# Optimization experiments

Hardware: AMD Instinct MI355X
Metric: run time of the kernel (lower is better)

## Reference

```python
import jax, jax.numpy as jnp
import numpy as np

NEG_SLOPE = 0.2


def gat_conv(x, src, dst, W, a_src, a_dst, bias, heads, out_ch):
    """PyG-style GATConv (concat=True, self-loops already appended)."""
    N = x.shape[0]
    h = (x @ W).reshape(N, heads, out_ch)            # [N,H,C]
    al_s = jnp.einsum('nhc,hc->nh', h, a_src)        # [N,H]
    al_d = jnp.einsum('nhc,hc->nh', h, a_dst)        # [N,H]
    e = al_s[src] + al_d[dst]                        # [E,H]
    e = jnp.where(e > 0, e, NEG_SLOPE * e)           # leaky_relu
    # segment softmax over edges grouped by destination node
    m = jax.ops.segment_max(e, dst, num_segments=N)  # [N,H]
    ex = jnp.exp(e - m[dst])
    s = jax.ops.segment_sum(ex, dst, num_segments=N)
    alpha = ex / s[dst]                              # [E,H]
    msg = alpha[:, :, None] * h[src]                 # [E,H,C]
    out = jax.ops.segment_sum(msg, dst, num_segments=N)  # [N,H,C]
    return out.reshape(N, heads * out_ch) + bias


def setup_inputs() -> dict:
    key = jax.random.key(0)
    ks = jax.random.split(key, 10)
    N, E = 100000, 1600000
    return {
        'x': jax.random.normal(ks[0], (N, 4), dtype=jnp.float32),
        'edge_index': jax.random.randint(ks[1], (2, E), 0, N, dtype=jnp.int64),
        'W1': jax.random.normal(ks[2], (4, 32), dtype=jnp.float32) * 0.5,
        'a_src1': jax.random.normal(ks[3], (2, 16), dtype=jnp.float32) * 0.5,
        'a_dst1': jax.random.normal(ks[4], (2, 16), dtype=jnp.float32) * 0.5,
        'b1': jax.random.normal(ks[5], (32,), dtype=jnp.float32) * 0.1,
        'W2': jax.random.normal(ks[6], (32, 2), dtype=jnp.float32) * 0.2,
        'a_src2': jax.random.normal(ks[7], (1, 2), dtype=jnp.float32) * 0.5,
        'a_dst2': jax.random.normal(ks[8], (1, 2), dtype=jnp.float32) * 0.5,
        'b2': jax.random.normal(ks[9], (2,), dtype=jnp.float32) * 0.1,
    }


def reference(x, edge_index, W1, a_src1, a_dst1, b1, W2, a_src2, a_dst2, b2):
    N = x.shape[0]
    loop = jnp.arange(N, dtype=edge_index.dtype)     # add_self_loops=True
    src = jnp.concatenate([edge_index[0], loop])
    dst = jnp.concatenate([edge_index[1], loop])
    # dropout(p=0.6) is identity at inference
    h = gat_conv(x, src, dst, W1, a_src1, a_dst1, b1, heads=2, out_ch=16)
    h = jax.nn.elu(h)
    out = gat_conv(h, src, dst, W2, a_src2, a_dst2, b2, heads=1, out_ch=2)
    return out
```

## Files before the change

### kernel.cpp

```cpp
#include <hip/hip_runtime.h>
#include <hip/hip_fp16.h>
#include <math.h>

#define NEG_SLOPE 0.2f
#define SCAN_CHUNK 2048
#define ECLAMP 80.0f
#define BUCKET_SHIFT 8
#define BUCKET_MASK 255
#define EB_CHUNK 8192

__device__ __forceinline__ float lrelu(float e) {
    return e > 0.f ? e : NEG_SLOPE * e;
}

__global__ void k0_prep1(const float* __restrict__ x,
                         const float* __restrict__ W1,
                         const float* __restrict__ a_src1,
                         const float* __restrict__ a_dst1,
                         __half* __restrict__ h1,
                         float* __restrict__ as1,
                         float* __restrict__ ad1,
                         int N) {
    int t = blockIdx.x * blockDim.x + threadIdx.x;
    int n = t >> 5;
    int c = t & 31;
    if (n >= N) return;
    const float4 xv = reinterpret_cast<const float4*>(x)[n];
    float h = xv.x * W1[c] + xv.y * W1[32 + c] + xv.z * W1[64 + c] + xv.w * W1[96 + c];
    h1[n * 32 + c] = __float2half(h);
    float ts = h * a_src1[c];
    float td = h * a_dst1[c];
#pragma unroll
    for (int m = 8; m >= 1; m >>= 1) {
        ts += __shfl_xor(ts, m);
        td += __shfl_xor(td, m);
    }
    if ((c & 15) == 0) {
        int hh = c >> 4;
        as1[n * 2 + hh] = ts;
        ad1[n * 2 + hh] = td;
    }
}

__global__ void p1_hist(const int* __restrict__ dst, int* __restrict__ cmatT,
                        int E, int NB, int nblkE) {
    __shared__ int cnt[512];
    const int blk = blockIdx.x, tid = threadIdx.x;
    for (int b = tid; b < NB; b += 256) cnt[b] = 0;
    __syncthreads();
    int base = blk * EB_CHUNK;
    int end = min(base + EB_CHUNK, E);
    for (int e = base + tid; e < end; e += 256)
        atomicAdd(&cnt[dst[e] >> BUCKET_SHIFT], 1);
    __syncthreads();
    for (int b = tid; b < NB; b += 256)
        cmatT[(size_t)b * nblkE + blk] = cnt[b];
}

__global__ void k2a_partials(const int* __restrict__ in, int* __restrict__ bsum, int n) {
    __shared__ int ws[4];
    const int tid = threadIdx.x;
    const int lane = tid & 63, wid = tid >> 6;
    int base = blockIdx.x * SCAN_CHUNK + tid * 8;
    int lsum = 0;
#pragma unroll
    for (int i = 0; i < 8; ++i) {
        int idx = base + i;
        lsum += (idx < n) ? in[idx] : 0;
    }
#pragma unroll
    for (int m = 32; m >= 1; m >>= 1) lsum += __shfl_xor(lsum, m);
    if (lane == 0) ws[wid] = lsum;
    __syncthreads();
    if (tid == 0) bsum[blockIdx.x] = ws[0] + ws[1] + ws[2] + ws[3];
}

__global__ void k2b_scanb(const int* __restrict__ bsum, int* __restrict__ bscan, int nb) {
    __shared__ int wsum[16];
    const int tid = threadIdx.x;
    const int lane = tid & 63, wid = tid >> 6;
    int carry = 0;
    for (int base = 0; base < nb; base += 1024) {
        int i = base + tid;
        int v = (i < nb) ? bsum[i] : 0;
        int xx = v;
#pragma unroll
        for (int off = 1; off < 64; off <<= 1) {
            int t = __shfl_up(xx, off);
            if (lane >= off) xx += t;
        }
        if (lane == 63) wsum[wid] = xx;
        __syncthreads();
        int woff = 0;
        for (int w = 0; w < wid; ++w) woff += wsum[w];
        if (i < nb) bscan[i] = carry + woff + xx - v;
        int tot = 0;
        for (int w = 0; w < 16; ++w) tot += wsum[w];
        carry += tot;
        __syncthreads();
    }
}

__global__ void k2c_scan(const int* __restrict__ in, const int* __restrict__ bscan,
                         int* __restrict__ out, int n) {
    __shared__ int ws[4];
    const int tid = threadIdx.x;
    const int lane = tid & 63, wid = tid >> 6;
    int base = blockIdx.x * SCAN_CHUNK + tid * 8;
    int v[8], pre[8];
    int lsum = 0;
#pragma unroll
    for (int i = 0; i < 8; ++i) {
        int idx = base + i;
        v[i] = (idx < n) ? in[idx] : 0;
        pre[i] = lsum;
        lsum += v[i];
    }
    int xs = lsum;
#pragma unroll
    for (int off = 1; off < 64; off <<= 1) {
        int t = __shfl_up(xs, off);
        if (lane >= off) xs += t;
    }
    if (lane == 63) ws[wid] = xs;
    __syncthreads();
    int woff = 0;
    for (int w = 0; w < wid; ++w) woff += ws[w];
    int off0 = bscan[blockIdx.x] + woff + xs - lsum;
#pragma unroll
    for (int i = 0; i < 8; ++i) {
        int idx = base + i;
        if (idx < n) out[idx] = off0 + pre[i];
    }
}

__global__ void p3_scatter(const int* __restrict__ src, const int* __restrict__ dst,
                           const int* __restrict__ cscan, unsigned int* __restrict__ ebuf,
                           int E, int NB, int nblkE) {
    __shared__ int cur[512];
    const int blk = blockIdx.x, tid = threadIdx.x;
    for (int b = tid; b < NB; b += 256)
        cur[b] = cscan[(size_t)b * nblkE + blk];
    __syncthreads();
    int base = blk * EB_CHUNK;
    int end = min(base + EB_CHUNK, E);
    for (int e = base + tid; e < end; e += 256) {
        int d = dst[e];
        int b = d >> BUCKET_SHIFT;
        int pos = atomicAdd(&cur[b], 1);
        ebuf[pos] = (unsigned int)src[e] | ((unsigned int)(d & BUCKET_MASK) << 24);
    }
}

__global__ void p4_csr(const unsigned int* __restrict__ ebuf,
                       const int* __restrict__ cscan,
                       int* __restrict__ rp, int* __restrict__ esrt,
                       int N, int E, int NB, int nblkE) {
    __shared__ int degl[256];
    __shared__ int curl[256];
    __shared__ int wsum[4];
    const int b = blockIdx.x, tid = threadIdx.x;
    const int lane = tid & 63, wid = tid >> 6;
    int bstart = cscan[(size_t)b * nblkE];
    int bend = (b + 1 < NB) ? cscan[(size_t)(b + 1) * nblkE] : E;
    degl[tid] = 0;
    __syncthreads();
    for (int i = bstart + tid; i < bend; i += 256)
        atomicAdd(&degl[ebuf[i] >> 24], 1);
    __syncthreads();
    int v = degl[tid];
    int xs = v;
#pragma unroll
    for (int off = 1; off < 64; off <<= 1) {
        int t = __shfl_up(xs, off);
        if (lane >= off) xs += t;
    }
    if (lane == 63) wsum[wid] = xs;
    __syncthreads();
    int woff = 0;
    for (int w = 0; w < wid; ++w) woff += wsum[w];
    int excl = woff + xs - v;
    int node = (b << BUCKET_SHIFT) + tid;
    if (node < N) rp[node] = bstart + excl;
    curl[tid] = bstart + excl;
    if (b == 0 && tid == 0) rp[N] = E;
    __syncthreads();
    for (int i = bstart + tid; i < bend; i += 256) {
        unsigned int ev = ebuf[i];
        int dl = ev >> 24;
        int pos = atomicAdd(&curl[dl], 1);
        esrt[pos] = (int)(ev & 0x00FFFFFFu);
    }
}

__global__ void k4_layer1(const int* __restrict__ rp, const int* __restrict__ esrt,
                          const __half* __restrict__ h1, const float* __restrict__ as1,
                          const float* __restrict__ ad1, const float* __restrict__ b1,
                          const float* __restrict__ W2, const float* __restrict__ a_src2,
                          const float* __restrict__ a_dst2,
                          float4* __restrict__ h2p, float* __restrict__ ad2,
                          int N) {
    int t = blockIdx.x * blockDim.x + threadIdx.x;
    int n = t >> 5;
    int c = t & 31;
    if (n >= N) return;
    int hh = c >> 4;
    const float2* as1v = reinterpret_cast<const float2*>(as1);
    const float2* ad1v = reinterpret_cast<const float2*>(ad1);
    float2 adv = ad1v[n];
    float ad = hh ? adv.y : adv.x;
    float2 asv_self = as1v[n];
    float e_self = lrelu((hh ? asv_self.y : asv_self.x) + ad);
    float w_self = __expf(fminf(e_self, ECLAMP));
    float s0 = w_self, s1 = 0.f, s2 = 0.f, s3 = 0.f;
    float acc0 = w_self * __half2float(h1[n * 32 + c]);
    float acc1 = 0.f, acc2 = 0.f, acc3 = 0.f;

    int p0 = rp[n], p1 = rp[n + 1];
    int p = p0;
    for (; p + 3 < p1; p += 4) {
        int sa = esrt[p];
        int sb = esrt[p + 1];
        int sc_ = esrt[p + 2];
        int sd = esrt[p + 3];
        float2 va = as1v[sa];
        float2 vb = as1v[sb];
        float2 vc = as1v[sc_];
        float2 vd = as1v[sd];
        float ha = __half2float(h1[(size_t)sa * 32 + c]);
        float hb = __half2float(h1[(size_t)sb * 32 + c]);
        float hc = __half2float(h1[(size_t)sc_ * 32 + c]);
        float hd = __half2float(h1[(size_t)sd * 32 + c]);
        float pa = __expf(fminf(lrelu((hh ? va.y : va.x) + ad), ECLAMP));
        float pb = __expf(fminf(lrelu((hh ? vb.y : vb.x) + ad), ECLAMP));
        float pc = __expf(fminf(lrelu((hh ? vc.y : vc.x) + ad), ECLAMP));
        float pd = __expf(fminf(lrelu((hh ? vd.y : vd.x) + ad), ECLAMP));
        s0 += pa;   acc0 += pa * ha;
        s1 += pb;   acc1 += pb * hb;
        s2 += pc;   acc2 += pc * hc;
        s3 += pd;   acc3 += pd * hd;
    }
    for (; p < p1; ++p) {
        int sa = esrt[p];
        float2 va = as1v[sa];
        float ha = __half2float(h1[(size_t)sa * 32 + c]);
        float pa = __expf(fminf(lrelu((hh ? va.y : va.x) + ad), ECLAMP));
        s0 += pa;   acc0 += pa * ha;
    }
    float s = (s0 + s1) + (s2 + s3);
    float acc = (acc0 + acc1) + (acc2 + acc3);
    float o = acc / s + b1[c];
    o = o > 0.f ? o : expm1f(o);
    float t0 = o * W2[c * 2 + 0];
    float t1 = o * W2[c * 2 + 1];
#pragma unroll
    for (int msk = 16; msk >= 1; msk >>= 1) {
        t0 += __shfl_xor(t0, msk);
        t1 += __shfl_xor(t1, msk);
    }
    if (c == 0) {
        float as2v = t0 * a_src2[0] + t1 * a_src2[1];
        float ad2v = t0 * a_dst2[0] + t1 * a_dst2[1];
        h2p[n] = make_float4(t0, t1, as2v, 0.f);
        ad2[n] = ad2v;
    }
}

__global__ void k5_layer2(const int* __restrict__ rp, const int* __restrict__ esrt,
                          const float4* __restrict__ h2p, const float* __restrict__ ad2,
                          const float* __restrict__ b2,
                          float* __restrict__ out, int N) {
    int t = blockIdx.x * blockDim.x + threadIdx.x;
    int n = t >> 2;
    int sub = t & 3;
    if (n >= N) return;
    float ad = ad2[n];
    float s = 0.f, xx = 0.f, yy = 0.f;
    if (sub == 0) {
        float4 hv = h2p[n];
        float w = __expf(fminf(lrelu(hv.z + ad), ECLAMP));
        s = w; xx = w * hv.x; yy = w * hv.y;
    }
    int p0 = rp[n], p1 = rp[n + 1];
    for (int p = p0 + sub; p < p1; p += 4) {
        int sn = esrt[p];
        float4 hv = h2p[sn];
        float w = __expf(fminf(lrelu(hv.z + ad), ECLAMP));
        s += w; xx += w * hv.x; yy += w * hv.y;
    }
#pragma unroll
    for (int msk = 1; msk <= 2; msk <<= 1) {
        s  += __shfl_xor(s, msk);
        xx += __shfl_xor(xx, msk);
        yy += __shfl_xor(yy, msk);
    }
    if (sub == 0) {
        float2 o;
        o.x = xx / s + b2[0];
        o.y = yy / s + b2[1];
        reinterpret_cast<float2*>(out)[n] = o;
    }
}

extern "C" void kernel_launch(void* const* d_in, const int* in_sizes, int n_in,
                              void* d_out, int out_size, void* d_ws, size_t ws_size,
                              hipStream_t stream) {
    const float* x      = (const float*)d_in[0];
    const int*   ei     = (const int*)d_in[1];
    const float* W1     = (const float*)d_in[2];
    const float* a_src1 = (const float*)d_in[3];
    const float* a_dst1 = (const float*)d_in[4];
    const float* b1     = (const float*)d_in[5];
    const float* W2     = (const float*)d_in[6];
    const float* a_src2 = (const float*)d_in[7];
    const float* a_dst2 = (const float*)d_in[8];
    const float* b2     = (const float*)d_in[9];
    float* out = (float*)d_out;

    const int N = in_sizes[0] / 4;
    const int E = in_sizes[1] / 2;
    const int* srcp = ei;
    const int* dstp = ei + E;

    const int NB    = (N + BUCKET_MASK) >> BUCKET_SHIFT;
    const int nblkE = (E + EB_CHUNK - 1) / EB_CHUNK;
    const int M     = NB * nblkE;
    const int nb2   = (M + SCAN_CHUNK - 1) / SCAN_CHUNK;

    char* w = (char*)d_ws;
    __half* h1   = (__half*)w;  w += (size_t)N * 32 * sizeof(__half);
    float*  as1  = (float*)w;   w += (size_t)N * 2 * sizeof(float);
    float*  ad1  = (float*)w;   w += (size_t)N * 2 * sizeof(float);
    float4* h2p  = (float4*)w;  w += (size_t)N * sizeof(float4);
    float*  ad2  = (float*)w;   w += (size_t)N * sizeof(float);
    int* rp     = (int*)w;      w += (size_t)(N + 4) * sizeof(int);
    int* cmatT  = (int*)w;      w += (size_t)M * sizeof(int);
    int* cscan  = (int*)w;      w += (size_t)M * sizeof(int);
    int* bsum   = (int*)w;      w += (size_t)(nb2 + 4) * sizeof(int);
    int* bscan  = (int*)w;      w += (size_t)(nb2 + 4) * sizeof(int);
    unsigned int* ebuf = (unsigned int*)w;  w += (size_t)E * sizeof(unsigned int);
    int* esrt   = (int*)w;      w += (size_t)E * sizeof(int);

    const int BT = 256;
    k0_prep1<<<((size_t)N * 32 + BT - 1) / BT, BT, 0, stream>>>(
        x, W1, a_src1, a_dst1, h1, as1, ad1, N);
    p1_hist<<<nblkE, 256, 0, stream>>>(dstp, cmatT, E, NB, nblkE);
    k2a_partials<<<nb2, 256, 0, stream>>>(cmatT, bsum, M);
    k2b_scanb<<<1, 1024, 0, stream>>>(bsum, bscan, nb2);
    k2c_scan<<<nb2, 256, 0, stream>>>(cmatT, bscan, cscan, M);
    p3_scatter<<<nblkE, 256, 0, stream>>>(srcp, dstp, cscan, ebuf, E, NB, nblkE);
    p4_csr<<<NB, 256, 0, stream>>>(ebuf, cscan, rp, esrt, N, E, NB, nblkE);
    k4_layer1<<<((size_t)N * 32 + BT - 1) / BT, BT, 0, stream>>>(
        rp, esrt, h1, as1, ad1, b1, W2, a_src2, a_dst2, h2p, ad2, N);
    k5_layer2<<<((size_t)N * 4 + BT - 1) / BT, BT, 0, stream>>>(
        rp, esrt, h2p, ad2, b2, out, N);
}
```

Before: 211.3 us.

## Precompute layer-1 softmax weights and node max/sum inside CSR build kernel

The CSR bucket kernel now computes the per-edge attention logits for layer 1, takes a per-destination max with ordered-int atomics in shared memory, and stores fp16 exp weights per edge plus per-node max and sum. The layer-1 aggregation kernel then reads these precomputed weights instead of gathering as1 and evaluating exp 32 times per edge (once per channel lane). This removes redundant exp and gather work from the hot kernel, but it adds a 4-byte weight array per edge, more shared-memory atomics and larger shared usage in p4_csr, and weights rounded to fp16.

Result: slower. 224.4 us (+6.2%).

```diff
diff --git a/kernel.cpp b/kernel.cpp
--- a/kernel.cpp
+++ b/kernel.cpp
@@ -4,13 +4,22 @@
 
 #define NEG_SLOPE 0.2f
 #define SCAN_CHUNK 2048
-#define ECLAMP 80.0f
 #define BUCKET_SHIFT 8
 #define BUCKET_MASK 255
 #define EB_CHUNK 8192
+#define EL_CAP 4992
+#define FENC_NEGINF 0x007FFFFFu
 
 __device__ __forceinline__ float lrelu(float e) {
     return e > 0.f ? e : NEG_SLOPE * e;
+}
+__device__ __forceinline__ unsigned fenc(float f) {
+    unsigned u = __float_as_uint(f);
+    return (u & 0x80000000u) ? ~u : (u | 0x80000000u);
+}
+__device__ __forceinline__ float fdec(unsigned u) {
+    unsigned b = (u & 0x80000000u) ? (u & 0x7FFFFFFFu) : ~u;
+    return __uint_as_float(b);
 }
 
 __global__ void k0_prep1(const float* __restrict__ x,
@@ -154,19 +163,46 @@
 
 __global__ void p4_csr(const unsigned int* __restrict__ ebuf,
                        const int* __restrict__ cscan,
+                       const float* __restrict__ as1,
+                       const float* __restrict__ ad1,
                        int* __restrict__ rp, int* __restrict__ esrt,
+                       __half2* __restrict__ wgtH, float4* __restrict__ nst,
                        int N, int E, int NB, int nblkE) {
+    __shared__ float2 eL[EL_CAP];
+    __shared__ unsigned maxL[512];
+    __shared__ float ssumL[512];
     __shared__ int degl[256];
     __shared__ int curl[256];
+    __shared__ float2 adL[256];
     __shared__ int wsum[4];
     const int b = blockIdx.x, tid = threadIdx.x;
     const int lane = tid & 63, wid = tid >> 6;
+    const float2* as1v = reinterpret_cast<const float2*>(as1);
+    const float2* ad1v = reinterpret_cast<const float2*>(ad1);
     int bstart = cscan[(size_t)b * nblkE];
     int bend = (b + 1 < NB) ? cscan[(size_t)(b + 1) * nblkE] : E;
+    int node = (b << BUCKET_SHIFT) + tid;
     degl[tid] = 0;
-    __syncthreads();
-    for (int i = bstart + tid; i < bend; i += 256)
-        atomicAdd(&degl[ebuf[i] >> 24], 1);
+    maxL[tid] = FENC_NEGINF;
+    maxL[tid + 256] = FENC_NEGINF;
+    ssumL[tid] = 0.f;
+    ssumL[tid + 256] = 0.f;
+    adL[tid] = (node < N) ? ad1v[node] : make_float2(0.f, 0.f);
+    __syncthreads();
+    for (int i = bstart + tid; i < bend; i += 256) {
+        unsigned ev = ebuf[i];
+        int dl = ev >> 24;
+        int srcn = ev & 0x00FFFFFF;
+        atomicAdd(&degl[dl], 1);
+        float2 av = as1v[srcn];
+        float2 adv = adL[dl];
+        float e0 = lrelu(av.x + adv.x);
+        float e1 = lrelu(av.y + adv.y);
+        int sl = i - bstart;
+        if (sl < EL_CAP) eL[sl] = make_float2(e0, e1);
+        atomicMax(&maxL[dl * 2], fenc(e0));
+        atomicMax(&maxL[dl * 2 + 1], fenc(e1));
+    }
     __syncthreads();
     int v = degl[tid];
     int xs = v;
@@ -180,20 +216,42 @@
     int woff = 0;
     for (int w = 0; w < wid; ++w) woff += wsum[w];
     int excl = woff + xs - v;
-    int node = (b << BUCKET_SHIFT) + tid;
     if (node < N) rp[node] = bstart + excl;
     curl[tid] = bstart + excl;
     if (b == 0 && tid == 0) rp[N] = E;
     __syncthreads();
     for (int i = bstart + tid; i < bend; i += 256) {
-        unsigned int ev = ebuf[i];
+        unsigned ev = ebuf[i];
         int dl = ev >> 24;
+        int srcn = ev & 0x00FFFFFF;
+        int sl = i - bstart;
+        float2 e;
+        if (sl < EL_CAP) {
+            e = eL[sl];
+        } else {
+            float2 av = as1v[srcn];
+            float2 adv = adL[dl];
+            e = make_float2(lrelu(av.x + adv.x), lrelu(av.y + adv.y));
+        }
+        float m0 = fdec(maxL[dl * 2]);
+        float m1 = fdec(maxL[dl * 2 + 1]);
+        float w0 = __expf(e.x - m0);
+        float w1 = __expf(e.y - m1);
+        atomicAdd(&ssumL[dl * 2], w0);
+        atomicAdd(&ssumL[dl * 2 + 1], w1);
         int pos = atomicAdd(&curl[dl], 1);
-        esrt[pos] = (int)(ev & 0x00FFFFFFu);
-    }
+        esrt[pos] = srcn;
+        wgtH[pos] = __floats2half2_rn(w0, w1);
+    }
+    __syncthreads();
+    if (node < N)
+        nst[node] = make_float4(fdec(maxL[tid * 2]), fdec(maxL[tid * 2 + 1]),
+                                ssumL[tid * 2], ssumL[tid * 2 + 1]);
 }
 
 __global__ void k4_layer1(const int* __restrict__ rp, const int* __restrict__ esrt,
+                          const __half2* __restrict__ wgtH,
+                          const float4* __restrict__ nst,
                           const __half* __restrict__ h1, const float* __restrict__ as1,
                           const float* __restrict__ ad1, const float* __restrict__ b1,
                           const float* __restrict__ W2, const float* __restrict__ a_src2,
@@ -208,48 +266,49 @@
     const float2* as1v = reinterpret_cast<const float2*>(as1);
     const float2* ad1v = reinterpret_cast<const float2*>(ad1);
     float2 adv = ad1v[n];
-    float ad = hh ? adv.y : adv.x;
-    float2 asv_self = as1v[n];
-    float e_self = lrelu((hh ? asv_self.y : asv_self.x) + ad);
-    float w_self = __expf(fminf(e_self, ECLAMP));
-    float s0 = w_self, s1 = 0.f, s2 = 0.f, s3 = 0.f;
-    float acc0 = w_self * __half2float(h1[n * 32 + c]);
-    float acc1 = 0.f, acc2 = 0.f, acc3 = 0.f;
-
+    float2 asv = as1v[n];
+    float es = lrelu((hh ? asv.y : asv.x) + (hh ? adv.y : adv.x));
+    float h_self = __half2float(h1[(size_t)n * 32 + c]);
+    float4 ns = nst[n];
     int p0 = rp[n], p1 = rp[n + 1];
-    int p = p0;
-    for (; p + 3 < p1; p += 4) {
-        int sa = esrt[p];
-        int sb = esrt[p + 1];
-        int sc_ = esrt[p + 2];
-        int sd = esrt[p + 3];
-        float2 va = as1v[sa];
-        float2 vb = as1v[sb];
-        float2 vc = as1v[sc_];
-        float2 vd = as1v[sd];
-        float ha = __half2float(h1[(size_t)sa * 32 + c]);
-        float hb = __half2float(h1[(size_t)sb * 32 + c]);
-        float hc = __half2float(h1[(size_t)sc_ * 32 + c]);
-        float hd = __half2float(h1[(size_t)sd * 32 + c]);
-        float pa = __expf(fminf(lrelu((hh ? va.y : va.x) + ad), ECLAMP));
-        float pb = __expf(fminf(lrelu((hh ? vb.y : vb.x) + ad), ECLAMP));
-        float pc = __expf(fminf(lrelu((hh ? vc.y : vc.x) + ad), ECLAMP));
-        float pd = __expf(fminf(lrelu((hh ? vd.y : vd.x) + ad), ECLAMP));
-        s0 += pa;   acc0 += pa * ha;
-        s1 += pb;   acc1 += pb * hb;
-        s2 += pc;   acc2 += pc * hc;
-        s3 += pd;   acc3 += pd * hd;
-    }
-    for (; p < p1; ++p) {
-        int sa = esrt[p];
-        float2 va = as1v[sa];
-        float ha = __half2float(h1[(size_t)sa * 32 + c]);
-        float pa = __expf(fminf(lrelu((hh ? va.y : va.x) + ad), ECLAMP));
-        s0 += pa;   acc0 += pa * ha;
-    }
-    float s = (s0 + s1) + (s2 + s3);
-    float acc = (acc0 + acc1) + (acc2 + acc3);
-    float o = acc / s + b1[c];
+    float acc, stot;
+    if (p0 == p1) {
+        acc = h_self;
+        stot = 1.f;
+    } else {
+        float m = hh ? ns.y : ns.x;
+        float se = hh ? ns.w : ns.z;
+        float w_self = __expf(es - m);
+        stot = se + w_self;
+        float a0 = w_self * h_self, a1 = 0.f, a2 = 0.f, a3 = 0.f;
+        int p = p0;
+        for (; p + 3 < p1; p += 4) {
+            int sa = esrt[p];
+            int sb = esrt[p + 1];
+            int sc_ = esrt[p + 2];
+            int sd = esrt[p + 3];
+            __half2 wa = wgtH[p];
+            __half2 wb = wgtH[p + 1];
+            __half2 wc = wgtH[p + 2];
+            __half2 wd = wgtH[p + 3];
+            float ha = __half2float(h1[(size_t)sa * 32 + c]);
+            float hb = __half2float(h1[(size_t)sb * 32 + c]);
+            float hc = __half2float(h1[(size_t)sc_ * 32 + c]);
+            float hd = __half2float(h1[(size_t)sd * 32 + c]);
+            a0 += (hh ? __high2float(wa) : __low2float(wa)) * ha;
+            a1 += (hh ? __high2float(wb) : __low2float(wb)) * hb;
+            a2 += (hh ? __high2float(wc) : __low2float(wc)) * hc;
+            a3 += (hh ? __high2float(wd) : __low2float(wd)) * hd;
+        }
+        for (; p < p1; ++p) {
+            int sa = esrt[p];
+            __half2 wa = wgtH[p];
+            float ha = __half2float(h1[(size_t)sa * 32 + c]);
+            a0 += (hh ? __high2float(wa) : __low2float(wa)) * ha;
+        }
+        acc = (a0 + a1) + (a2 + a3);
+    }
+    float o = acc / stot + b1[c];
     o = o > 0.f ? o : expm1f(o);
     float t0 = o * W2[c * 2 + 0];
     float t1 = o * W2[c * 2 + 1];
@@ -278,14 +337,14 @@
     float s = 0.f, xx = 0.f, yy = 0.f;
     if (sub == 0) {
         float4 hv = h2p[n];
-        float w = __expf(fminf(lrelu(hv.z + ad), ECLAMP));
+        float w = __expf(fminf(lrelu(hv.z + ad), 80.f));
         s = w; xx = w * hv.x; yy = w * hv.y;
     }
     int p0 = rp[n], p1 = rp[n + 1];
     for (int p = p0 + sub; p < p1; p += 4) {
         int sn = esrt[p];
         float4 hv = h2p[sn];
-        float w = __expf(fminf(lrelu(hv.z + ad), ECLAMP));
+        float w = __expf(fminf(lrelu(hv.z + ad), 80.f));
         s += w; xx += w * hv.x; yy += w * hv.y;
     }
 #pragma unroll
@@ -333,6 +392,7 @@
     float*  ad1  = (float*)w;   w += (size_t)N * 2 * sizeof(float);
     float4* h2p  = (float4*)w;  w += (size_t)N * sizeof(float4);
     float*  ad2  = (float*)w;   w += (size_t)N * sizeof(float);
+    float4* nst  = (float4*)w;  w += (size_t)N * sizeof(float4);
     int* rp     = (int*)w;      w += (size_t)(N + 4) * sizeof(int);
     int* cmatT  = (int*)w;      w += (size_t)M * sizeof(int);
     int* cscan  = (int*)w;      w += (size_t)M * sizeof(int);
@@ -340,6 +400,7 @@
     int* bscan  = (int*)w;      w += (size_t)(nb2 + 4) * sizeof(int);
     unsigned int* ebuf = (unsigned int*)w;  w += (size_t)E * sizeof(unsigned int);
     int* esrt   = (int*)w;      w += (size_t)E * sizeof(int);
+    __half2* wgtH = (__half2*)w; w += (size_t)E * sizeof(__half2);
 
     const int BT = 256;
     k0_prep1<<<((size_t)N * 32 + BT - 1) / BT, BT, 0, stream>>>(
@@ -349,9 +410,10 @@
     k2b_scanb<<<1, 1024, 0, stream>>>(bsum, bscan, nb2);
     k2c_scan<<<nb2, 256, 0, stream>>>(cmatT, bscan, cscan, M);
     p3_scatter<<<nblkE, 256, 0, stream>>>(srcp, dstp, cscan, ebuf, E, NB, nblkE);
-    p4_csr<<<NB, 256, 0, stream>>>(ebuf, cscan, rp, esrt, N, E, NB, nblkE);
+    p4_csr<<<NB, 256, 0, stream>>>(ebuf, cscan, as1, ad1, rp, esrt, wgtH, nst,
+                                   N, E, NB, nblkE);
     k4_layer1<<<((size_t)N * 32 + BT - 1) / BT, BT, 0, stream>>>(
-        rp, esrt, h1, as1, ad1, b1, W2, a_src2, a_dst2, h2p, ad2, N);
+        rp, esrt, wgtH, nst, h1, as1, ad1, b1, W2, a_src2, a_dst2, h2p, ad2, N);
     k5_layer2<<<((size_t)N * 4 + BT - 1) / BT, BT, 0, stream>>>(
         rp, esrt, h2p, ad2, b2, out, N);
 }
```

## Aggregate raw 4-dim inputs in layer 1 and apply W1 after aggregation

Applied to the files above, without the earlier changes.

Uses linearity: since h = xW1, the attention-weighted sum of h[src] equals W1 applied to the weighted sum of x[src]. Layer 1 now gathers 4-float x rows per head instead of 32-wide fp16 h1 rows, runs 8 threads per node instead of 32, and no longer materialises h1 in the prep kernel. This cuts gather traffic and thread count in the dominant edge loop. The cost is a small per-node matmul after aggregation and a slightly different rounding order.

Result: faster. 179.2 us (-15.2%).

```diff
diff --git a/kernel.cpp b/kernel.cpp
--- a/kernel.cpp
+++ b/kernel.cpp
@@ -1,5 +1,4 @@
 #include <hip/hip_runtime.h>
-#include <hip/hip_fp16.h>
 #include <math.h>
 
 #define NEG_SLOPE 0.2f
@@ -17,7 +16,6 @@
                          const float* __restrict__ W1,
                          const float* __restrict__ a_src1,
                          const float* __restrict__ a_dst1,
-                         __half* __restrict__ h1,
                          float* __restrict__ as1,
                          float* __restrict__ ad1,
                          int N) {
@@ -27,7 +25,6 @@
     if (n >= N) return;
     const float4 xv = reinterpret_cast<const float4*>(x)[n];
     float h = xv.x * W1[c] + xv.y * W1[32 + c] + xv.z * W1[64 + c] + xv.w * W1[96 + c];
-    h1[n * 32 + c] = __float2half(h);
     float ts = h * a_src1[c];
     float td = h * a_dst1[c];
 #pragma unroll
@@ -194,27 +191,24 @@
 }
 
 __global__ void k4_layer1(const int* __restrict__ rp, const int* __restrict__ esrt,
-                          const __half* __restrict__ h1, const float* __restrict__ as1,
+                          const float* __restrict__ x, const float* __restrict__ as1,
                           const float* __restrict__ ad1, const float* __restrict__ b1,
+                          const float* __restrict__ W1,
                           const float* __restrict__ W2, const float* __restrict__ a_src2,
                           const float* __restrict__ a_dst2,
                           float4* __restrict__ h2p, float* __restrict__ ad2,
                           int N) {
     int t = blockIdx.x * blockDim.x + threadIdx.x;
-    int n = t >> 5;
-    int c = t & 31;
+    int n = t >> 3;
+    int l = t & 7;
     if (n >= N) return;
-    int hh = c >> 4;
-    const float2* as1v = reinterpret_cast<const float2*>(as1);
-    const float2* ad1v = reinterpret_cast<const float2*>(ad1);
-    float2 adv = ad1v[n];
-    float ad = hh ? adv.y : adv.x;
-    float2 asv_self = as1v[n];
-    float e_self = lrelu((hh ? asv_self.y : asv_self.x) + ad);
-    float w_self = __expf(fminf(e_self, ECLAMP));
-    float s0 = w_self, s1 = 0.f, s2 = 0.f, s3 = 0.f;
-    float acc0 = w_self * __half2float(h1[n * 32 + c]);
-    float acc1 = 0.f, acc2 = 0.f, acc3 = 0.f;
+    int h = l >> 2;
+    int d = l & 3;
+    float ad = ad1[n * 2 + h];
+    float es = lrelu(as1[n * 2 + h] + ad);
+    float ws = __expf(fminf(es, ECLAMP));
+    float g0 = ws * x[(size_t)n * 4 + d], g1 = 0.f, g2 = 0.f, g3 = 0.f;
+    float s0 = ws, s1 = 0.f, s2 = 0.f, s3 = 0.f;
 
     int p0 = rp[n], p1 = rp[n + 1];
     int p = p0;
@@ -223,42 +217,58 @@
         int sb = esrt[p + 1];
         int sc_ = esrt[p + 2];
         int sd = esrt[p + 3];
-        float2 va = as1v[sa];
-        float2 vb = as1v[sb];
-        float2 vc = as1v[sc_];
-        float2 vd = as1v[sd];
-        float ha = __half2float(h1[(size_t)sa * 32 + c]);
-        float hb = __half2float(h1[(size_t)sb * 32 + c]);
-        float hc = __half2float(h1[(size_t)sc_ * 32 + c]);
-        float hd = __half2float(h1[(size_t)sd * 32 + c]);
-        float pa = __expf(fminf(lrelu((hh ? va.y : va.x) + ad), ECLAMP));
-        float pb = __expf(fminf(lrelu((hh ? vb.y : vb.x) + ad), ECLAMP));
-        float pc = __expf(fminf(lrelu((hh ? vc.y : vc.x) + ad), ECLAMP));
-        float pd = __expf(fminf(lrelu((hh ? vd.y : vd.x) + ad), ECLAMP));
-        s0 += pa;   acc0 += pa * ha;
-        s1 += pb;   acc1 += pb * hb;
-        s2 += pc;   acc2 += pc * hc;
-        s3 += pd;   acc3 += pd * hd;
+        float ea = lrelu(as1[(size_t)sa * 2 + h] + ad);
+        float eb = lrelu(as1[(size_t)sb * 2 + h] + ad);
+        float ec = lrelu(as1[(size_t)sc_ * 2 + h] + ad);
+        float ed = lrelu(as1[(size_t)sd * 2 + h] + ad);
+        float xa = x[(size_t)sa * 4 + d];
+        float xb = x[(size_t)sb * 4 + d];
+        float xc = x[(size_t)sc_ * 4 + d];
+        float xd = x[(size_t)sd * 4 + d];
+        float wa = __expf(fminf(ea, ECLAMP));
+        float wb = __expf(fminf(eb, ECLAMP));
+        float wc = __expf(fminf(ec, ECLAMP));
+        float wd = __expf(fminf(ed, ECLAMP));
+        s0 += wa;  g0 += wa * xa;
+        s1 += wb;  g1 += wb * xb;
+        s2 += wc;  g2 += wc * xc;
+        s3 += wd;  g3 += wd * xd;
     }
     for (; p < p1; ++p) {
         int sa = esrt[p];
-        float2 va = as1v[sa];
-        float ha = __half2float(h1[(size_t)sa * 32 + c]);
-        float pa = __expf(fminf(lrelu((hh ? va.y : va.x) + ad), ECLAMP));
-        s0 += pa;   acc0 += pa * ha;
+        float ea = lrelu(as1[(size_t)sa * 2 + h] + ad);
+        float xa = x[(size_t)sa * 4 + d];
+        float wa = __expf(fminf(ea, ECLAMP));
+        s0 += wa;  g0 += wa * xa;
     }
     float s = (s0 + s1) + (s2 + s3);
-    float acc = (acc0 + acc1) + (acc2 + acc3);
-    float o = acc / s + b1[c];
-    o = o > 0.f ? o : expm1f(o);
-    float t0 = o * W2[c * 2 + 0];
-    float t1 = o * W2[c * 2 + 1];
-#pragma unroll
-    for (int msk = 16; msk >= 1; msk >>= 1) {
+    float agg = ((g0 + g1) + (g2 + g3)) / s;
+
+    float a2[2][4];
+#pragma unroll
+    for (int k = 0; k < 8; ++k)
+        a2[k >> 2][k & 3] = __shfl(agg, k, 8);
+
+    float t0 = 0.f, t1 = 0.f;
+#pragma unroll
+    for (int j = 0; j < 4; ++j) {
+        int c = l * 4 + j;
+        int hc = c >> 4;
+        float o = b1[c]
+                + a2[hc][0] * W1[c]
+                + a2[hc][1] * W1[32 + c]
+                + a2[hc][2] * W1[64 + c]
+                + a2[hc][3] * W1[96 + c];
+        o = o > 0.f ? o : expm1f(o);
+        t0 += o * W2[c * 2 + 0];
+        t1 += o * W2[c * 2 + 1];
+    }
+#pragma unroll
+    for (int msk = 1; msk <= 4; msk <<= 1) {
         t0 += __shfl_xor(t0, msk);
         t1 += __shfl_xor(t1, msk);
     }
-    if (c == 0) {
+    if (l == 0) {
         float as2v = t0 * a_src2[0] + t1 * a_src2[1];
         float ad2v = t0 * a_dst2[0] + t1 * a_dst2[1];
         h2p[n] = make_float4(t0, t1, as2v, 0.f);
@@ -328,10 +338,9 @@
     const int nb2   = (M + SCAN_CHUNK - 1) / SCAN_CHUNK;
 
     char* w = (char*)d_ws;
-    __half* h1   = (__half*)w;  w += (size_t)N * 32 * sizeof(__half);
+    float4* h2p  = (float4*)w;  w += (size_t)N * sizeof(float4);
     float*  as1  = (float*)w;   w += (size_t)N * 2 * sizeof(float);
     float*  ad1  = (float*)w;   w += (size_t)N * 2 * sizeof(float);
-    float4* h2p  = (float4*)w;  w += (size_t)N * sizeof(float4);
     float*  ad2  = (float*)w;   w += (size_t)N * sizeof(float);
     int* rp     = (int*)w;      w += (size_t)(N + 4) * sizeof(int);
     int* cmatT  = (int*)w;      w += (size_t)M * sizeof(int);
@@ -343,15 +352,15 @@
 
     const int BT = 256;
     k0_prep1<<<((size_t)N * 32 + BT - 1) / BT, BT, 0, stream>>>(
-        x, W1, a_src1, a_dst1, h1, as1, ad1, N);
+        x, W1, a_src1, a_dst1, as1, ad1, N);
     p1_hist<<<nblkE, 256, 0, stream>>>(dstp, cmatT, E, NB, nblkE);
     k2a_partials<<<nb2, 256, 0, stream>>>(cmatT, bsum, M);
     k2b_scanb<<<1, 1024, 0, stream>>>(bsum, bscan, nb2);
     k2c_scan<<<nb2, 256, 0, stream>>>(cmatT, bscan, cscan, M);
     p3_scatter<<<nblkE, 256, 0, stream>>>(srcp, dstp, cscan, ebuf, E, NB, nblkE);
     p4_csr<<<NB, 256, 0, stream>>>(ebuf, cscan, rp, esrt, N, E, NB, nblkE);
-    k4_layer1<<<((size_t)N * 32 + BT - 1) / BT, BT, 0, stream>>>(
-        rp, esrt, h1, as1, ad1, b1, W2, a_src2, a_dst2, h2p, ad2, N);
+    k4_layer1<<<((size_t)N * 8 + BT - 1) / BT, BT, 0, stream>>>(
+        rp, esrt, x, as1, ad1, b1, W1, W2, a_src2, a_dst2, h2p, ad2, N);
     k5_layer2<<<((size_t)N * 4 + BT - 1) / BT, BT, 0, stream>>>(
         rp, esrt, h2p, ad2, b2, out, N);
 }
```

## Aggregate raw 4-dim inputs per bucket and drop CSR build for layers

Applied to the files above, without the earlier changes.

Layer 1 no longer gathers the 32-wide hidden features. Because h = x@W1 is linear, it accumulates attention-weighted 4-dim x rows per destination node in shared memory with atomics, then applies W1 after aggregation. Both layers now consume the bucketed edge buffer directly using per-bucket shared-memory atomics, which removes the per-node CSR build kernel, the esrt and rp arrays, and the h1 buffer. Bucket size is halved to 128 nodes. In exchange, shared-memory float atomics may contend on high-degree nodes, and summation order is no longer deterministic.

Measured after the change: 274.8 us. +30.1%, slower.

```diff
diff --git a/kernel.cpp b/kernel.cpp
--- a/kernel.cpp
+++ b/kernel.cpp
@@ -1,13 +1,14 @@
 #include <hip/hip_runtime.h>
-#include <hip/hip_fp16.h>
 #include <math.h>
 
 #define NEG_SLOPE 0.2f
 #define SCAN_CHUNK 2048
 #define ECLAMP 80.0f
-#define BUCKET_SHIFT 8
-#define BUCKET_MASK 255
-#define EB_CHUNK 8192
+#define BUCKET_SHIFT 7
+#define BUCKET_MASK 127
+#define NPB 128
+#define NBMAX 1024
+#define EB_CHUNK 4096
 
 __device__ __forceinline__ float lrelu(float e) {
     return e > 0.f ? e : NEG_SLOPE * e;
@@ -17,7 +18,6 @@
                          const float* __restrict__ W1,
                          const float* __restrict__ a_src1,
                          const float* __restrict__ a_dst1,
-                         __half* __restrict__ h1,
                          float* __restrict__ as1,
                          float* __restrict__ ad1,
                          int N) {
@@ -27,7 +27,6 @@
     if (n >= N) return;
     const float4 xv = reinterpret_cast<const float4*>(x)[n];
     float h = xv.x * W1[c] + xv.y * W1[32 + c] + xv.z * W1[64 + c] + xv.w * W1[96 + c];
-    h1[n * 32 + c] = __float2half(h);
     float ts = h * a_src1[c];
     float td = h * a_dst1[c];
 #pragma unroll
@@ -44,7 +43,7 @@
 
 __global__ void p1_hist(const int* __restrict__ dst, int* __restrict__ cmatT,
                         int E, int NB, int nblkE) {
-    __shared__ int cnt[512];
+    __shared__ int cnt[NBMAX];
     const int blk = blockIdx.x, tid = threadIdx.x;
     for (int b = tid; b < NB; b += 256) cnt[b] = 0;
     __syncthreads();
@@ -137,7 +136,7 @@
 __global__ void p3_scatter(const int* __restrict__ src, const int* __restrict__ dst,
                            const int* __restrict__ cscan, unsigned int* __restrict__ ebuf,
                            int E, int NB, int nblkE) {
-    __shared__ int cur[512];
+    __shared__ int cur[NBMAX];
     const int blk = blockIdx.x, tid = threadIdx.x;
     for (int b = tid; b < NB; b += 256)
         cur[b] = cscan[(size_t)b * nblkE + blk];
@@ -152,153 +151,130 @@
     }
 }
 
-__global__ void p4_csr(const unsigned int* __restrict__ ebuf,
-                       const int* __restrict__ cscan,
-                       int* __restrict__ rp, int* __restrict__ esrt,
-                       int N, int E, int NB, int nblkE) {
-    __shared__ int degl[256];
-    __shared__ int curl[256];
-    __shared__ int wsum[4];
+__global__ void a1_layer1(const unsigned int* __restrict__ ebuf,
+                          const int* __restrict__ cscan,
+                          const float* __restrict__ x, const float* __restrict__ as1,
+                          const float* __restrict__ ad1, const float* __restrict__ b1,
+                          const float* __restrict__ W1, const float* __restrict__ W2,
+                          const float* __restrict__ a_src2, const float* __restrict__ a_dst2,
+                          float4* __restrict__ h2p, float* __restrict__ ad2,
+                          int N, int E, int NB, int nblkE) {
+    __shared__ float acc[NPB][10];
+    __shared__ float2 adL[NPB];
     const int b = blockIdx.x, tid = threadIdx.x;
-    const int lane = tid & 63, wid = tid >> 6;
+    const float2* as1v = reinterpret_cast<const float2*>(as1);
+    const float2* ad1v = reinterpret_cast<const float2*>(ad1);
+    const float4* x4 = reinterpret_cast<const float4*>(x);
     int bstart = cscan[(size_t)b * nblkE];
     int bend = (b + 1 < NB) ? cscan[(size_t)(b + 1) * nblkE] : E;
-    degl[tid] = 0;
-    __syncthreads();
-    for (int i = bstart + tid; i < bend; i += 256)
-        atomicAdd(&degl[ebuf[i] >> 24], 1);
-    __syncthreads();
-    int v = degl[tid];
-    int xs = v;
-#pragma unroll
-    for (int off = 1; off < 64; off <<= 1) {
-        int t = __shfl_up(xs, off);
-        if (lane >= off) xs += t;
-    }
-    if (lane == 63) wsum[wid] = xs;
-    __syncthreads();
-    int woff = 0;
-    for (int w = 0; w < wid; ++w) woff += wsum[w];
-    int excl = woff + xs - v;
-    int node = (b << BUCKET_SHIFT) + tid;
-    if (node < N) rp[node] = bstart + excl;
-    curl[tid] = bstart + excl;
-    if (b == 0 && tid == 0) rp[N] = E;
+    int node0 = b << BUCKET_SHIFT;
+    if (tid < NPB) {
+#pragma unroll
+        for (int k = 0; k < 10; ++k) acc[tid][k] = 0.f;
+        int node = node0 + tid;
+        adL[tid] = (node < N) ? ad1v[node] : make_float2(0.f, 0.f);
+    }
     __syncthreads();
     for (int i = bstart + tid; i < bend; i += 256) {
         unsigned int ev = ebuf[i];
         int dl = ev >> 24;
-        int pos = atomicAdd(&curl[dl], 1);
-        esrt[pos] = (int)(ev & 0x00FFFFFFu);
-    }
-}
-
-__global__ void k4_layer1(const int* __restrict__ rp, const int* __restrict__ esrt,
-                          const __half* __restrict__ h1, const float* __restrict__ as1,
-                          const float* __restrict__ ad1, const float* __restrict__ b1,
-                          const float* __restrict__ W2, const float* __restrict__ a_src2,
-                          const float* __restrict__ a_dst2,
-                          float4* __restrict__ h2p, float* __restrict__ ad2,
-                          int N) {
-    int t = blockIdx.x * blockDim.x + threadIdx.x;
-    int n = t >> 5;
-    int c = t & 31;
-    if (n >= N) return;
-    int hh = c >> 4;
-    const float2* as1v = reinterpret_cast<const float2*>(as1);
-    const float2* ad1v = reinterpret_cast<const float2*>(ad1);
-    float2 adv = ad1v[n];
-    float ad = hh ? adv.y : adv.x;
-    float2 asv_self = as1v[n];
-    float e_self = lrelu((hh ? asv_self.y : asv_self.x) + ad);
-    float w_self = __expf(fminf(e_self, ECLAMP));
-    float s0 = w_self, s1 = 0.f, s2 = 0.f, s3 = 0.f;
-    float acc0 = w_self * __half2float(h1[n * 32 + c]);
-    float acc1 = 0.f, acc2 = 0.f, acc3 = 0.f;
-
-    int p0 = rp[n], p1 = rp[n + 1];
-    int p = p0;
-    for (; p + 3 < p1; p += 4) {
-        int sa = esrt[p];
-        int sb = esrt[p + 1];
-        int sc_ = esrt[p + 2];
-        int sd = esrt[p + 3];
-        float2 va = as1v[sa];
-        float2 vb = as1v[sb];
-        float2 vc = as1v[sc_];
-        float2 vd = as1v[sd];
-        float ha = __half2float(h1[(size_t)sa * 32 + c]);
-        float hb = __half2float(h1[(size_t)sb * 32 + c]);
-        float hc = __half2float(h1[(size_t)sc_ * 32 + c]);
-        float hd = __half2float(h1[(size_t)sd * 32 + c]);
-        float pa = __expf(fminf(lrelu((hh ? va.y : va.x) + ad), ECLAMP));
-        float pb = __expf(fminf(lrelu((hh ? vb.y : vb.x) + ad), ECLAMP));
-        float pc = __expf(fminf(lrelu((hh ? vc.y : vc.x) + ad), ECLAMP));
-        float pd = __expf(fminf(lrelu((hh ? vd.y : vd.x) + ad), ECLAMP));
-        s0 += pa;   acc0 += pa * ha;
-        s1 += pb;   acc1 += pb * hb;
-        s2 += pc;   acc2 += pc * hc;
-        s3 += pd;   acc3 += pd * hd;
-    }
-    for (; p < p1; ++p) {
-        int sa = esrt[p];
-        float2 va = as1v[sa];
-        float ha = __half2float(h1[(size_t)sa * 32 + c]);
-        float pa = __expf(fminf(lrelu((hh ? va.y : va.x) + ad), ECLAMP));
-        s0 += pa;   acc0 += pa * ha;
-    }
-    float s = (s0 + s1) + (s2 + s3);
-    float acc = (acc0 + acc1) + (acc2 + acc3);
-    float o = acc / s + b1[c];
-    o = o > 0.f ? o : expm1f(o);
-    float t0 = o * W2[c * 2 + 0];
-    float t1 = o * W2[c * 2 + 1];
-#pragma unroll
-    for (int msk = 16; msk >= 1; msk >>= 1) {
-        t0 += __shfl_xor(t0, msk);
-        t1 += __shfl_xor(t1, msk);
-    }
-    if (c == 0) {
-        float as2v = t0 * a_src2[0] + t1 * a_src2[1];
-        float ad2v = t0 * a_dst2[0] + t1 * a_dst2[1];
-        h2p[n] = make_float4(t0, t1, as2v, 0.f);
-        ad2[n] = ad2v;
-    }
-}
-
-__global__ void k5_layer2(const int* __restrict__ rp, const int* __restrict__ esrt,
+        int srcn = ev & 0x00FFFFFF;
+        float2 av = as1v[srcn];
+        float4 xv = x4[srcn];
+        float2 adv = adL[dl];
+        float w0 = __expf(fminf(lrelu(av.x + adv.x), ECLAMP));
+        float w1 = __expf(fminf(lrelu(av.y + adv.y), ECLAMP));
+        float* a = acc[dl];
+        atomicAdd(&a[0], w0);
+        atomicAdd(&a[1], w0 * xv.x);
+        atomicAdd(&a[2], w0 * xv.y);
+        atomicAdd(&a[3], w0 * xv.z);
+        atomicAdd(&a[4], w0 * xv.w);
+        atomicAdd(&a[5], w1);
+        atomicAdd(&a[6], w1 * xv.x);
+        atomicAdd(&a[7], w1 * xv.y);
+        atomicAdd(&a[8], w1 * xv.z);
+        atomicAdd(&a[9], w1 * xv.w);
+    }
+    __syncthreads();
+    if (tid < NPB) {
+        int n = node0 + tid;
+        if (n < N) {
+            float2 asv = as1v[n];
+            float2 adv = adL[tid];
+            float4 xv = x4[n];
+            float w0 = __expf(fminf(lrelu(asv.x + adv.x), ECLAMP));
+            float w1 = __expf(fminf(lrelu(asv.y + adv.y), ECLAMP));
+            float s0 = acc[tid][0] + w0;
+            float s1 = acc[tid][5] + w1;
+            float ag[2][4];
+            ag[0][0] = (acc[tid][1] + w0 * xv.x) / s0;
+            ag[0][1] = (acc[tid][2] + w0 * xv.y) / s0;
+            ag[0][2] = (acc[tid][3] + w0 * xv.z) / s0;
+            ag[0][3] = (acc[tid][4] + w0 * xv.w) / s0;
+            ag[1][0] = (acc[tid][6] + w1 * xv.x) / s1;
+            ag[1][1] = (acc[tid][7] + w1 * xv.y) / s1;
+            ag[1][2] = (acc[tid][8] + w1 * xv.z) / s1;
+            ag[1][3] = (acc[tid][9] + w1 * xv.w) / s1;
+            float t0 = 0.f, t1 = 0.f;
+#pragma unroll
+            for (int c = 0; c < 32; ++c) {
+                const float* g = ag[c >> 4];
+                float o = b1[c] + g[0] * W1[c] + g[1] * W1[32 + c]
+                        + g[2] * W1[64 + c] + g[3] * W1[96 + c];
+                o = o > 0.f ? o : expm1f(o);
+                t0 += o * W2[c * 2 + 0];
+                t1 += o * W2[c * 2 + 1];
+            }
+            float as2v = t0 * a_src2[0] + t1 * a_src2[1];
+            float ad2v = t0 * a_dst2[0] + t1 * a_dst2[1];
+            h2p[n] = make_float4(t0, t1, as2v, 0.f);
+            ad2[n] = ad2v;
+        }
+    }
+}
+
+__global__ void a2_layer2(const unsigned int* __restrict__ ebuf,
+                          const int* __restrict__ cscan,
                           const float4* __restrict__ h2p, const float* __restrict__ ad2,
                           const float* __restrict__ b2,
-                          float* __restrict__ out, int N) {
-    int t = blockIdx.x * blockDim.x + threadIdx.x;
-    int n = t >> 2;
-    int sub = t & 3;
-    if (n >= N) return;
-    float ad = ad2[n];
-    float s = 0.f, xx = 0.f, yy = 0.f;
-    if (sub == 0) {
-        float4 hv = h2p[n];
-        float w = __expf(fminf(lrelu(hv.z + ad), ECLAMP));
-        s = w; xx = w * hv.x; yy = w * hv.y;
-    }
-    int p0 = rp[n], p1 = rp[n + 1];
-    for (int p = p0 + sub; p < p1; p += 4) {
-        int sn = esrt[p];
-        float4 hv = h2p[sn];
-        float w = __expf(fminf(lrelu(hv.z + ad), ECLAMP));
-        s += w; xx += w * hv.x; yy += w * hv.y;
-    }
-#pragma unroll
-    for (int msk = 1; msk <= 2; msk <<= 1) {
-        s  += __shfl_xor(s, msk);
-        xx += __shfl_xor(xx, msk);
-        yy += __shfl_xor(yy, msk);
-    }
-    if (sub == 0) {
-        float2 o;
-        o.x = xx / s + b2[0];
-        o.y = yy / s + b2[1];
-        reinterpret_cast<float2*>(out)[n] = o;
+                          float* __restrict__ out,
+                          int N, int E, int NB, int nblkE) {
+    __shared__ float acc[NPB][3];
+    __shared__ float adL[NPB];
+    const int b = blockIdx.x, tid = threadIdx.x;
+    int bstart = cscan[(size_t)b * nblkE];
+    int bend = (b + 1 < NB) ? cscan[(size_t)(b + 1) * nblkE] : E;
+    int node0 = b << BUCKET_SHIFT;
+    if (tid < NPB) {
+        acc[tid][0] = 0.f; acc[tid][1] = 0.f; acc[tid][2] = 0.f;
+        int node = node0 + tid;
+        adL[tid] = (node < N) ? ad2[node] : 0.f;
+    }
+    __syncthreads();
+    for (int i = bstart + tid; i < bend; i += 256) {
+        unsigned int ev = ebuf[i];
+        int dl = ev >> 24;
+        int srcn = ev & 0x00FFFFFF;
+        float4 hv = h2p[srcn];
+        float w = __expf(fminf(lrelu(hv.z + adL[dl]), ECLAMP));
+        float* a = acc[dl];
+        atomicAdd(&a[0], w);
+        atomicAdd(&a[1], w * hv.x);
+        atomicAdd(&a[2], w * hv.y);
+    }
+    __syncthreads();
+    if (tid < NPB) {
+        int n = node0 + tid;
+        if (n < N) {
+            float4 hv = h2p[n];
+            float w = __expf(fminf(lrelu(hv.z + adL[tid]), ECLAMP));
+            float s = acc[tid][0] + w;
+            float2 o;
+            o.x = (acc[tid][1] + w * hv.x) / s + b2[0];
+            o.y = (acc[tid][2] + w * hv.y) / s + b2[1];
+            reinterpret_cast<float2*>(out)[n] = o;
+        }
     }
 }
 
@@ -328,30 +304,25 @@
     const int nb2   = (M + SCAN_CHUNK - 1) / SCAN_CHUNK;
 
     char* w = (char*)d_ws;
-    __half* h1   = (__half*)w;  w += (size_t)N * 32 * sizeof(__half);
+    float4* h2p  = (float4*)w;  w += (size_t)N * sizeof(float4);
     float*  as1  = (float*)w;   w += (size_t)N * 2 * sizeof(float);
     float*  ad1  = (float*)w;   w += (size_t)N * 2 * sizeof(float);
-    float4* h2p  = (float4*)w;  w += (size_t)N * sizeof(float4);
     float*  ad2  = (float*)w;   w += (size_t)N * sizeof(float);
-    int* rp     = (int*)w;      w += (size_t)(N + 4) * sizeof(int);
     int* cmatT  = (int*)w;      w += (size_t)M * sizeof(int);
     int* cscan  = (int*)w;      w += (size_t)M * sizeof(int);
     int* bsum   = (int*)w;      w += (size_t)(nb2 + 4) * sizeof(int);
     int* bscan  = (int*)w;      w += (size_t)(nb2 + 4) * sizeof(int);
     unsigned int* ebuf = (unsigned int*)w;  w += (size_t)E * sizeof(unsigned int);
-    int* esrt   = (int*)w;      w += (size_t)E * sizeof(int);
 
     const int BT = 256;
     k0_prep1<<<((size_t)N * 32 + BT - 1) / BT, BT, 0, stream>>>(
-        x, W1, a_src1, a_dst1, h1, as1, ad1, N);
+        x, W1, a_src1, a_dst1, as1, ad1, N);
     p1_hist<<<nblkE, 256, 0, stream>>>(dstp, cmatT, E, NB, nblkE);
     k2a_partials<<<nb2, 256, 0, stream>>>(cmatT, bsum, M);
     k2b_scanb<<<1, 1024, 0, stream>>>(bsum, bscan, nb2);
     k2c_scan<<<nb2, 256, 0, stream>>>(cmatT, bscan, cscan, M);
     p3_scatter<<<nblkE, 256, 0, stream>>>(srcp, dstp, cscan, ebuf, E, NB, nblkE);
-    p4_csr<<<NB, 256, 0, stream>>>(ebuf, cscan, rp, esrt, N, E, NB, nblkE);
-    k4_layer1<<<((size_t)N * 32 + BT - 1) / BT, BT, 0, stream>>>(
-        rp, esrt, h1, as1, ad1, b1, W2, a_src2, a_dst2, h2p, ad2, N);
-    k5_layer2<<<((size_t)N * 4 + BT - 1) / BT, BT, 0, stream>>>(
-        rp, esrt, h2p, ad2, b2, out, N);
-}
+    a1_layer1<<<NB, 256, 0, stream>>>(ebuf, cscan, x, as1, ad1, b1, W1, W2,
+                                      a_src2, a_dst2, h2p, ad2, N, E, NB, nblkE);
+    a2_layer2<<<NB, 256, 0, stream>>>(ebuf, cscan, h2p, ad2, b2, out, N, E, NB, nblkE);
+}
```
